# Optimization experiments

Hardware: AMD Instinct MI355X
Metric: run time of the kernel (lower is better)

The kernel has to match this reference:

```python
import jax, jax.numpy as jnp
import numpy as np

T, IN, OUT, R = 8192, 4096, 4096, 64


def setup_inputs() -> dict:
    key = jax.random.key(0)
    ks = jax.random.split(key, 7)
    # signed int4 values in [-8, 8) for activations and (unpacked) weights
    quant_x = jax.random.randint(ks[0], (T, IN), -8, 8, dtype=jnp.int32)
    weight_q = jax.random.randint(ks[1], (OUT, IN), -8, 8, dtype=jnp.int32)
    # positive per-token / per-channel symmetric-quant scales
    scale_x = jax.random.uniform(ks[2], (T,), dtype=jnp.float32) * 0.01 + 1e-4
    weight_scales = jax.random.uniform(ks[3], (OUT,), dtype=jnp.float32) * 0.01 + 1e-4
    outlier_x = jax.random.normal(ks[4], (T, R), dtype=jnp.float32)
    w_outlier = jax.random.normal(ks[5], (OUT, R), dtype=jnp.float32)
    bias = jax.random.normal(ks[6], (OUT,), dtype=jnp.float32)
    return {"quant_x": quant_x, "weight_q": weight_q, "scale_x": scale_x,
            "weight_scales": weight_scales, "outlier_x": outlier_x,
            "w_outlier": w_outlier, "bias": bias}


def reference(quant_x, weight_q, scale_x, weight_scales, outlier_x, w_outlier, bias):
    acc = jnp.matmul(quant_x, weight_q.T)
    # sym_dequant: per-row activation scale * per-column weight scale
    x_out = acc.astype(jnp.float32) * scale_x[:, None] * weight_scales[None, :]
    # outlier low-rank addmm + bias epilogue
    x_out = x_out + jnp.matmul(outlier_x, w_outlier.T) + bias
    return x_out
```

## Files before the change

### kernel.cpp

```cpp
#include <hip/hip_runtime.h>

#define T_DIM 8192
#define IN_DIM 4096
#define OUT_DIM 4096
#define R_DIM 64
#define NKT 64

typedef int i32x4 __attribute__((ext_vector_type(4)));
typedef float f32x4 __attribute__((ext_vector_type(4)));
typedef _Float16 f16x8 __attribute__((ext_vector_type(8)));

__device__ __forceinline__ int pack4(int4 v) {
  return (v.x & 255) | ((v.y & 255) << 8) | ((v.z & 255) << 16) | ((unsigned)v.w << 24);
}

__device__ __forceinline__ void gload16(const void* g, void* l) {
  __builtin_amdgcn_global_load_lds(
      (const __attribute__((address_space(1))) void*)(unsigned long long)g,
      (__attribute__((address_space(3))) void*)(unsigned)(unsigned long long)l,
      16, 0, 0);
}

__device__ __forceinline__ i32x4 unp(int x, int y) {
  i32x4 r;
  r[0] = x & 0x0F0F0F0F;
  r[1] = (x >> 4) & 0x0F0F0F0F;
  r[2] = y & 0x0F0F0F0F;
  r[3] = (y >> 4) & 0x0F0F0F0F;
  return r;
}

__device__ __forceinline__ unsigned pb(int a, int b) {
  return (unsigned)(a + 8) | ((unsigned)(b + 8) << 4);
}

__global__ __launch_bounds__(256)
void cvt_pack_kernel(const int* __restrict__ qx, const int* __restrict__ wq,
                     char* __restrict__ pk, int* __restrict__ SS) {
  const int wave = blockIdx.x * 4 + (threadIdx.x >> 6);
  const int l = threadIdx.x & 63;
  const int nw = gridDim.x * 4;
  for (int r = wave; r < T_DIM + OUT_DIM; r += nw) {
    const int* src = (r < T_DIM) ? (qx + (size_t)r * IN_DIM)
                                 : (wq + (size_t)(r - T_DIM) * IN_DIM);
    const int4* src4 = (const int4*)src;
    char* dst = pk + (size_t)r * 2048;
    const int rq = (r >> 2) & 3;
    int s = 0;
#pragma unroll
    for (int i = 0; i < 4; ++i) {
      const int idx = i * 64 + l;
      const int kt = idx >> 2, d = idx & 3;
      int4 s0 = src4[idx * 4 + 0], s1 = src4[idx * 4 + 1];
      int4 s2 = src4[idx * 4 + 2], s3 = src4[idx * 4 + 3];
      s += s0.x + s0.y + s0.z + s0.w + s1.x + s1.y + s1.z + s1.w +
           s2.x + s2.y + s2.z + s2.w + s3.x + s3.y + s3.z + s3.w;
      unsigned dw0 = pb(s0.x, s0.y) | (pb(s0.z, s0.w) << 8) |
                     (pb(s1.x, s1.y) << 16) | (pb(s1.z, s1.w) << 24);
      unsigned dw1 = pb(s2.x, s2.y) | (pb(s2.z, s2.w) << 8) |
                     (pb(s3.x, s3.y) << 16) | (pb(s3.z, s3.w) << 24);
      const int off = kt * 32 + ((d ^ rq) << 3);
      *(uint2*)(dst + off) = make_uint2(dw0, dw1);
    }
#pragma unroll
    for (int off = 1; off < 64; off <<= 1) s += __shfl_xor(s, off, 64);
    if (l == 0) SS[r] = s + 8 * IN_DIM;
  }
}

__global__ __launch_bounds__(256, 4)
void w4a4_gemm(const char* __restrict__ A8, const char* __restrict__ B8,
               const int* __restrict__ SS,
               const float* __restrict__ sx, const float* __restrict__ sw,
               const float* __restrict__ ox, const float* __restrict__ ow,
               const float* __restrict__ bias, float* __restrict__ out) {
  __shared__ __align__(16) char smem[32768];

  const int bid = blockIdx.x;
  const int xcd = bid & 7, c = bid >> 3;
  const int tn = (xcd & 3) * 8 + (c & 7);
  const int tm = (xcd >> 2) * 32 + (c >> 3);
  const int brow = tm * 128, bcol = tn * 128;

  const int t = threadIdx.x;
  const int w = t >> 6, l = t & 63;
  const int wr = w >> 1, wc = w & 1;
  const int l16 = l & 15, lk = l >> 4;
  (void)w;

  const char* gA = A8 + (size_t)(brow + (t >> 1)) * 2048 + (t & 1) * 16;
  const char* gB = B8 + (size_t)(bcol + (t >> 1)) * 2048 + (t & 1) * 16;
  char* const dA = smem + t * 16;
  char* const dB = smem + 4096 + t * 16;

  const int cho = (lk ^ ((l16 >> 2) & 3)) << 3;
  const char* aR = smem + (wr * 64 + l16) * 32 + cho;
  const char* bR = smem + 4096 + (wc * 64 + l16) * 32 + cho;

  i32x4 acc[4][4];
#pragma unroll
  for (int m = 0; m < 4; ++m)
#pragma unroll
    for (int n = 0; n < 4; ++n) acc[m][n] = (i32x4){0, 0, 0, 0};

  auto stage = [&](int kt) {
    const int off = kt << 5;
    const int buf = (kt & 3) << 13;
    gload16(gA + off, dA + buf);
    gload16(gB + off, dB + buf);
  };

  auto compute = [&](int kt) {
    const int buf = (kt & 3) << 13;
    const char* sa = aR + buf;
    const char* sb = bR + buf;
    int2 pa[4], pv[4];
#pragma unroll
    for (int m = 0; m < 4; ++m) pa[m] = *(const int2*)(sa + m * 512);
#pragma unroll
    for (int n = 0; n < 4; ++n) pv[n] = *(const int2*)(sb + n * 512);
    i32x4 bu[4];
#pragma unroll
    for (int n = 0; n < 4; ++n) bu[n] = unp(pv[n].x, pv[n].y);
    __builtin_amdgcn_s_setprio(1);
#pragma unroll
    for (int m = 0; m < 4; ++m) {
      i32x4 au = unp(pa[m].x, pa[m].y);
      acc[m][0] = __builtin_amdgcn_mfma_i32_16x16x64_i8(au, bu[0], acc[m][0], 0, 0, 0);
      acc[m][1] = __builtin_amdgcn_mfma_i32_16x16x64_i8(au, bu[1], acc[m][1], 0, 0, 0);
      acc[m][2] = __builtin_amdgcn_mfma_i32_16x16x64_i8(au, bu[2], acc[m][2], 0, 0, 0);
      acc[m][3] = __builtin_amdgcn_mfma_i32_16x16x64_i8(au, bu[3], acc[m][3], 0, 0, 0);
    }
    __builtin_amdgcn_s_setprio(0);
  };

#define VMBAR(N)                                          \
  asm volatile("s_waitcnt vmcnt(" #N ")" ::: "memory");   \
  __builtin_amdgcn_s_barrier();                           \
  __builtin_amdgcn_sched_barrier(0);

  stage(0); stage(1); stage(2);
  for (int kt = 0; kt < NKT - 3; ++kt) {
    VMBAR(4);
    stage(kt + 3);
    compute(kt);
  }
  VMBAR(4);
  compute(NKT - 3);
  VMBAR(2);
  compute(NKT - 2);
  VMBAR(0);
  compute(NKT - 1);

  const int orow0 = brow + wr * 64 + (lk << 2);
  const int ocol0 = bcol + wc * 64 + l16;
  const int* SA = SS;
  const int* SB = SS + T_DIM;
  float swv[4], bvv[4];
  int cb[4];
#pragma unroll
  for (int n = 0; n < 4; ++n) {
    swv[n] = sw[ocol0 + n * 16];
    bvv[n] = bias[ocol0 + n * 16];
    cb[n] = -8 * SB[ocol0 + n * 16];
  }

  f32x4 facc[4][4];
#pragma unroll
  for (int m = 0; m < 4; ++m) {
#pragma unroll
    for (int r = 0; r < 4; ++r) {
      const int row = orow0 + m * 16 + r;
      const float sxv = sx[row];
      const int ca = 262144 - 8 * SA[row];
#pragma unroll
      for (int n = 0; n < 4; ++n)
        facc[m][n][r] = (float)(acc[m][n][r] + ca + cb[n]) * sxv * swv[n];
    }
  }

  __syncthreads();
#pragma unroll
  for (int j = 0; j < 4; ++j) {
    int q = j * 256 + t;
    int row = q >> 3, cd = q & 7, cs = cd ^ (row & 7);
    const float* ga = ox + (size_t)(brow + row) * R_DIM + cs * 8;
    float4 f0 = *(const float4*)ga, f1 = *(const float4*)(ga + 4);
    f16x8 h;
    h[0] = (_Float16)f0.x; h[1] = (_Float16)f0.y; h[2] = (_Float16)f0.z; h[3] = (_Float16)f0.w;
    h[4] = (_Float16)f1.x; h[5] = (_Float16)f1.y; h[6] = (_Float16)f1.z; h[7] = (_Float16)f1.w;
    *(f16x8*)(smem + row * 128 + cd * 16) = h;
    const float* gb = ow + (size_t)(bcol + row) * R_DIM + cs * 8;
    f0 = *(const float4*)gb; f1 = *(const float4*)(gb + 4);
    f16x8 g;
    g[0] = (_Float16)f0.x; g[1] = (_Float16)f0.y; g[2] = (_Float16)f0.z; g[3] = (_Float16)f0.w;
    g[4] = (_Float16)f1.x; g[5] = (_Float16)f1.y; g[6] = (_Float16)f1.z; g[7] = (_Float16)f1.w;
    *(f16x8*)(smem + 16384 + row * 128 + cd * 16) = g;
  }
  __syncthreads();

  const char* qa = smem + (wr * 64 + l16) * 128;
  const char* qb = smem + 16384 + (wc * 64 + l16) * 128;
  const int x7 = l16 & 7;
#pragma unroll
  for (int s = 0; s < 2; ++s) {
    const int ca2 = ((s * 4 + lk) ^ x7) << 4;
    f16x8 hb[4];
#pragma unroll
    for (int n = 0; n < 4; ++n) hb[n] = *(const f16x8*)(qb + n * 2048 + ca2);
#pragma unroll
    for (int m = 0; m < 4; ++m) {
      f16x8 ha = *(const f16x8*)(qa + m * 2048 + ca2);
#pragma unroll
      for (int n = 0; n < 4; ++n)
        facc[m][n] = __builtin_amdgcn_mfma_f32_16x16x32_f16(ha, hb[n], facc[m][n], 0, 0, 0);
    }
  }

#pragma unroll
  for (int m = 0; m < 4; ++m)
#pragma unroll
    for (int r = 0; r < 4; ++r) {
      float* po = out + (size_t)(orow0 + m * 16 + r) * OUT_DIM + ocol0;
#pragma unroll
      for (int n = 0; n < 4; ++n) po[n * 16] = facc[m][n][r] + bvv[n];
    }
}

__global__ __launch_bounds__(256)
void w4a4_gemm_fb(const int* __restrict__ A32, const int* __restrict__ B32,
                  const float* __restrict__ sx, const float* __restrict__ sw,
                  const float* __restrict__ ox, const float* __restrict__ ow,
                  const float* __restrict__ bias, float* __restrict__ out) {
  __shared__ __align__(16) unsigned char smem[32768];
  char* sA = (char*)smem;
  char* sB = (char*)smem + 8192;

  const int bid = blockIdx.x;
  const int swzb = (bid & 7) * 256 + (bid >> 3);
  const int tm = swzb >> 5, tn = swzb & 31;
  const int brow = tm * 128, bcol = tn * 128;

  const int t = threadIdx.x;
  const int l = t & 63;
  const int wr = (t >> 6) >> 1, wc = (t >> 6) & 1;
  const int l16 = l & 15, lk = l >> 4;

  i32x4 iacc[4][4];
#pragma unroll
  for (int m = 0; m < 4; ++m)
#pragma unroll
    for (int n = 0; n < 4; ++n) iacc[m][n] = (i32x4){0, 0, 0, 0};

  const int ar = t >> 2;
  const int ac = (t & 3) << 4;
  const int* hA0 = A32 + (size_t)(brow + ar) * IN_DIM + ac;
  const int* hA1 = hA0 + (size_t)64 * IN_DIM;
  const int* hB0 = B32 + (size_t)(bcol + ar) * IN_DIM + ac;
  const int* hB1 = hB0 + (size_t)64 * IN_DIM;

  const char* fragA = sA + (size_t)(wr * 64 + l16) * 64 + lk * 16;
  const char* fragB = sB + (size_t)(wc * 64 + l16) * 64 + lk * 16;

  for (int k0 = 0; k0 < IN_DIM; k0 += 64) {
    const int4* pA0 = (const int4*)(hA0 + k0);
    int4 r0 = {pack4(pA0[0]), pack4(pA0[1]), pack4(pA0[2]), pack4(pA0[3])};
    *(int4*)(sA + t * 16) = r0;
    const int4* pA1 = (const int4*)(hA1 + k0);
    int4 r1 = {pack4(pA1[0]), pack4(pA1[1]), pack4(pA1[2]), pack4(pA1[3])};
    *(int4*)(sA + 4096 + t * 16) = r1;
    const int4* pB0 = (const int4*)(hB0 + k0);
    int4 r2 = {pack4(pB0[0]), pack4(pB0[1]), pack4(pB0[2]), pack4(pB0[3])};
    *(int4*)(sB + t * 16) = r2;
    const int4* pB1 = (const int4*)(hB1 + k0);
    int4 r3 = {pack4(pB1[0]), pack4(pB1[1]), pack4(pB1[2]), pack4(pB1[3])};
    *(int4*)(sB + 4096 + t * 16) = r3;
    __syncthreads();
    i32x4 av[4], bv[4];
#pragma unroll
    for (int m = 0; m < 4; ++m) av[m] = *(const i32x4*)(fragA + m * 1024);
#pragma unroll
    for (int n = 0; n < 4; ++n) bv[n] = *(const i32x4*)(fragB + n * 1024);
#pragma unroll
    for (int m = 0; m < 4; ++m)
#pragma unroll
      for (int n = 0; n < 4; ++n)
        iacc[m][n] = __builtin_amdgcn_mfma_i32_16x16x64_i8(av[m], bv[n], iacc[m][n], 0, 0, 0);
    __syncthreads();
  }

  const int orow = brow + wr * 64 + lk * 4;
  const int ocol = bcol + wc * 64 + l16;
  float swv[4], bvv[4];
#pragma unroll
  for (int n = 0; n < 4; ++n) { swv[n] = sw[ocol + n * 16]; bvv[n] = bias[ocol + n * 16]; }

  f32x4 facc[4][4];
#pragma unroll
  for (int m = 0; m < 4; ++m)
#pragma unroll
    for (int r = 0; r < 4; ++r) {
      float sxv = sx[orow + m * 16 + r];
#pragma unroll
      for (int n = 0; n < 4; ++n) facc[m][n][r] = (float)iacc[m][n][r] * sxv * swv[n];
    }

  _Float16* oA = (_Float16*)smem;
  _Float16* oB = (_Float16*)(smem + 16384);
#pragma unroll
  for (int j = 0; j < 4; ++j) {
    int c = j * 256 + t;
    int rr2 = c >> 3, c8 = (c & 7) << 3;
    const float* gp = ox + (size_t)(brow + rr2) * R_DIM + c8;
    float4 f0 = *(const float4*)gp;
    float4 f1 = *(const float4*)(gp + 4);
    f16x8 h;
    h[0] = (_Float16)f0.x; h[1] = (_Float16)f0.y; h[2] = (_Float16)f0.z; h[3] = (_Float16)f0.w;
    h[4] = (_Float16)f1.x; h[5] = (_Float16)f1.y; h[6] = (_Float16)f1.z; h[7] = (_Float16)f1.w;
    *(f16x8*)((char*)oA + (size_t)c * 16) = h;
    const float* gq = ow + (size_t)(bcol + rr2) * R_DIM + c8;
    f0 = *(const float4*)gq; f1 = *(const float4*)(gq + 4);
    f16x8 g;
    g[0] = (_Float16)f0.x; g[1] = (_Float16)f0.y; g[2] = (_Float16)f0.z; g[3] = (_Float16)f0.w;
    g[4] = (_Float16)f1.x; g[5] = (_Float16)f1.y; g[6] = (_Float16)f1.z; g[7] = (_Float16)f1.w;
    *(f16x8*)((char*)oB + (size_t)c * 16) = g;
  }
  __syncthreads();

  const char* qa = (const char*)oA + (size_t)(wr * 64 + l16) * 128 + lk * 16;
  const char* qb = (const char*)oB + (size_t)(wc * 64 + l16) * 128 + lk * 16;
#pragma unroll
  for (int s = 0; s < 2; ++s) {
    f16x8 ha[4], hb[4];
#pragma unroll
    for (int m = 0; m < 4; ++m) ha[m] = *(const f16x8*)(qa + m * 2048 + s * 64);
#pragma unroll
    for (int n = 0; n < 4; ++n) hb[n] = *(const f16x8*)(qb + n * 2048 + s * 64);
#pragma unroll
    for (int m = 0; m < 4; ++m)
#pragma unroll
      for (int n = 0; n < 4; ++n)
        facc[m][n] = __builtin_amdgcn_mfma_f32_16x16x32_f16(ha[m], hb[n], facc[m][n], 0, 0, 0);
  }

#pragma unroll
  for (int m = 0; m < 4; ++m)
#pragma unroll
    for (int r = 0; r < 4; ++r) {
      float* po = out + (size_t)(orow + m * 16 + r) * OUT_DIM + ocol;
#pragma unroll
      for (int n = 0; n < 4; ++n) po[n * 16] = facc[m][n][r] + bvv[n];
    }
}

extern "C" void kernel_launch(void* const* d_in, const int* in_sizes, int n_in,
                              void* d_out, int out_size, void* d_ws, size_t ws_size,
                              hipStream_t stream) {
  const int*   qx   = (const int*)d_in[0];
  const int*   wq   = (const int*)d_in[1];
  const float* sx   = (const float*)d_in[2];
  const float* sw   = (const float*)d_in[3];
  const float* ox   = (const float*)d_in[4];
  const float* ow   = (const float*)d_in[5];
  const float* bias = (const float*)d_in[6];
  float* out = (float*)d_out;

  const size_t packedA = (size_t)T_DIM * 2048;
  const size_t packedB = (size_t)OUT_DIM * 2048;
  const size_t ssBytes = (size_t)(T_DIM + OUT_DIM) * 4;
  const size_t need = packedA + packedB + ssBytes;

  if (ws_size >= need) {
    char* pk = (char*)d_ws;
    int* SS = (int*)(pk + packedA + packedB);
    cvt_pack_kernel<<<768, 256, 0, stream>>>(qx, wq, pk, SS);
    w4a4_gemm<<<2048, 256, 0, stream>>>(pk, pk + packedA, SS, sx, sw, ox, ow, bias, out);
  } else {
    w4a4_gemm_fb<<<2048, 256, 0, stream>>>(qx, wq, sx, sw, ox, ow, bias, out);
  }
}
```

Baseline: 204.2 us.

## Pre-swizzle packed operands into MFMA fragment order and load directly to registers

The pack kernel now writes the int4 operands already laid out in per-wave MFMA fragment order (64-row blocks, per k-tile), so the GEMM drops the LDS staging, barriers and async global-to-LDS pipeline. Each wave instead double-buffers global loads straight into registers. Occupancy hint drops to 2 blocks per CU. Row sums are now reduced across four blocks with atomics, which needs an extra zeroing kernel. The risk is that global-load latency and L2 traffic are no longer shared through LDS across waves, and the added launch costs time.

Measured after the change: 203.0 us. Within noise of the previous version (-0.6%).

```diff
diff --git a/kernel.cpp b/kernel.cpp
--- a/kernel.cpp
+++ b/kernel.cpp
@@ -4,7 +4,6 @@
 #define IN_DIM 4096
 #define OUT_DIM 4096
 #define R_DIM 64
-#define NKT 64
 
 typedef int i32x4 __attribute__((ext_vector_type(4)));
 typedef float f32x4 __attribute__((ext_vector_type(4)));
@@ -12,13 +11,6 @@
 
 __device__ __forceinline__ int pack4(int4 v) {
   return (v.x & 255) | ((v.y & 255) << 8) | ((v.z & 255) << 16) | ((unsigned)v.w << 24);
-}
-
-__device__ __forceinline__ void gload16(const void* g, void* l) {
-  __builtin_amdgcn_global_load_lds(
-      (const __attribute__((address_space(1))) void*)(unsigned long long)g,
-      (__attribute__((address_space(3))) void*)(unsigned)(unsigned long long)l,
-      16, 0, 0);
 }
 
 __device__ __forceinline__ i32x4 unp(int x, int y) {
@@ -34,42 +26,61 @@
   return (unsigned)(a + 8) | ((unsigned)(b + 8) << 4);
 }
 
+__global__ __launch_bounds__(1024)
+void ss_zero_kernel(int* __restrict__ SS) {
+  SS[blockIdx.x * 1024 + threadIdx.x] = 0;
+}
+
 __global__ __launch_bounds__(256)
 void cvt_pack_kernel(const int* __restrict__ qx, const int* __restrict__ wq,
                      char* __restrict__ pk, int* __restrict__ SS) {
-  const int wave = blockIdx.x * 4 + (threadIdx.x >> 6);
-  const int l = threadIdx.x & 63;
-  const int nw = gridDim.x * 4;
-  for (int r = wave; r < T_DIM + OUT_DIM; r += nw) {
-    const int* src = (r < T_DIM) ? (qx + (size_t)r * IN_DIM)
-                                 : (wq + (size_t)(r - T_DIM) * IN_DIM);
-    const int4* src4 = (const int4*)src;
-    char* dst = pk + (size_t)r * 2048;
-    const int rq = (r >> 2) & 3;
-    int s = 0;
-#pragma unroll
-    for (int i = 0; i < 4; ++i) {
-      const int idx = i * 64 + l;
-      const int kt = idx >> 2, d = idx & 3;
-      int4 s0 = src4[idx * 4 + 0], s1 = src4[idx * 4 + 1];
-      int4 s2 = src4[idx * 4 + 2], s3 = src4[idx * 4 + 3];
-      s += s0.x + s0.y + s0.z + s0.w + s1.x + s1.y + s1.z + s1.w +
-           s2.x + s2.y + s2.z + s2.w + s3.x + s3.y + s3.z + s3.w;
-      unsigned dw0 = pb(s0.x, s0.y) | (pb(s0.z, s0.w) << 8) |
-                     (pb(s1.x, s1.y) << 16) | (pb(s1.z, s1.w) << 24);
-      unsigned dw1 = pb(s2.x, s2.y) | (pb(s2.z, s2.w) << 8) |
-                     (pb(s3.x, s3.y) << 16) | (pb(s3.z, s3.w) << 24);
-      const int off = kt * 32 + ((d ^ rq) << 3);
-      *(uint2*)(dst + off) = make_uint2(dw0, dw1);
-    }
-#pragma unroll
-    for (int off = 1; off < 64; off <<= 1) s += __shfl_xor(s, off, 64);
-    if (l == 0) SS[r] = s + 8 * IN_DIM;
-  }
-}
-
-__global__ __launch_bounds__(256, 4)
-void w4a4_gemm(const char* __restrict__ A8, const char* __restrict__ B8,
+  const int rb = blockIdx.x >> 2;
+  const int q = blockIdx.x & 3;
+  const int w = threadIdx.x >> 6, l = threadIdx.x & 63;
+  const int l16 = l & 15, lk = l >> 4;
+
+  const int* src = (rb < 128) ? (qx + (size_t)rb * 64 * IN_DIM)
+                              : (wq + (size_t)(rb - 128) * 64 * IN_DIM);
+  char* dst = pk + (size_t)rb * 131072;
+
+  int s[4] = {0, 0, 0, 0};
+#pragma unroll
+  for (int j = 0; j < 4; ++j) {
+    const int kt = q * 16 + w * 4 + j;
+#pragma unroll
+    for (int m = 0; m < 4; ++m) {
+      const int row = m * 16 + l16;
+      const int4* ip = (const int4*)((const char*)src + (size_t)row * 16384 + kt * 256 + lk * 64);
+      int4 v0 = ip[0], v1 = ip[1], v2 = ip[2], v3 = ip[3];
+      s[m] += v0.x + v0.y + v0.z + v0.w + v1.x + v1.y + v1.z + v1.w +
+              v2.x + v2.y + v2.z + v2.w + v3.x + v3.y + v3.z + v3.w;
+      unsigned dw0 = pb(v0.x, v0.y) | (pb(v0.z, v0.w) << 8) |
+                     (pb(v1.x, v1.y) << 16) | (pb(v1.z, v1.w) << 24);
+      unsigned dw1 = pb(v2.x, v2.y) | (pb(v2.z, v2.w) << 8) |
+                     (pb(v3.x, v3.y) << 16) | (pb(v3.z, v3.w) << 24);
+      *(uint2*)(dst + kt * 2048 + m * 512 + l * 8) = make_uint2(dw0, dw1);
+    }
+  }
+
+  __shared__ int sPart[256];
+#pragma unroll
+  for (int m = 0; m < 4; ++m) {
+    int v = s[m];
+    v += __shfl_xor(v, 16, 64);
+    v += __shfl_xor(v, 32, 64);
+    if (l < 16) sPart[w * 64 + m * 16 + l] = v;
+  }
+  __syncthreads();
+  const int t = threadIdx.x;
+  if (t < 64) {
+    int tot = sPart[t] + sPart[64 + t] + sPart[128 + t] + sPart[192 + t];
+    if (q == 0) tot += 8 * IN_DIM;
+    atomicAdd(&SS[rb * 64 + t], tot);
+  }
+}
+
+__global__ __launch_bounds__(256, 2)
+void w4a4_gemm(const char* __restrict__ A2, const char* __restrict__ B2,
                const int* __restrict__ SS,
                const float* __restrict__ sx, const float* __restrict__ sw,
                const float* __restrict__ ox, const float* __restrict__ ow,
@@ -86,16 +97,9 @@
   const int w = t >> 6, l = t & 63;
   const int wr = w >> 1, wc = w & 1;
   const int l16 = l & 15, lk = l >> 4;
-  (void)w;
-
-  const char* gA = A8 + (size_t)(brow + (t >> 1)) * 2048 + (t & 1) * 16;
-  const char* gB = B8 + (size_t)(bcol + (t >> 1)) * 2048 + (t & 1) * 16;
-  char* const dA = smem + t * 16;
-  char* const dB = smem + 4096 + t * 16;
-
-  const int cho = (lk ^ ((l16 >> 2) & 3)) << 3;
-  const char* aR = smem + (wr * 64 + l16) * 32 + cho;
-  const char* bR = smem + 4096 + (wc * 64 + l16) * 32 + cho;
+
+  const char* aP = A2 + (size_t)(tm * 2 + wr) * 131072 + l * 8;
+  const char* bP = B2 + (size_t)(tn * 2 + wc) * 131072 + l * 8;
 
   i32x4 acc[4][4];
 #pragma unroll
@@ -103,54 +107,50 @@
 #pragma unroll
     for (int n = 0; n < 4; ++n) acc[m][n] = (i32x4){0, 0, 0, 0};
 
-  auto stage = [&](int kt) {
-    const int off = kt << 5;
-    const int buf = (kt & 3) << 13;
-    gload16(gA + off, dA + buf);
-    gload16(gB + off, dB + buf);
-  };
-
-  auto compute = [&](int kt) {
-    const int buf = (kt & 3) << 13;
-    const char* sa = aR + buf;
-    const char* sb = bR + buf;
-    int2 pa[4], pv[4];
-#pragma unroll
-    for (int m = 0; m < 4; ++m) pa[m] = *(const int2*)(sa + m * 512);
-#pragma unroll
-    for (int n = 0; n < 4; ++n) pv[n] = *(const int2*)(sb + n * 512);
-    i32x4 bu[4];
-#pragma unroll
-    for (int n = 0; n < 4; ++n) bu[n] = unp(pv[n].x, pv[n].y);
-    __builtin_amdgcn_s_setprio(1);
-#pragma unroll
-    for (int m = 0; m < 4; ++m) {
-      i32x4 au = unp(pa[m].x, pa[m].y);
-      acc[m][0] = __builtin_amdgcn_mfma_i32_16x16x64_i8(au, bu[0], acc[m][0], 0, 0, 0);
-      acc[m][1] = __builtin_amdgcn_mfma_i32_16x16x64_i8(au, bu[1], acc[m][1], 0, 0, 0);
-      acc[m][2] = __builtin_amdgcn_mfma_i32_16x16x64_i8(au, bu[2], acc[m][2], 0, 0, 0);
-      acc[m][3] = __builtin_amdgcn_mfma_i32_16x16x64_i8(au, bu[3], acc[m][3], 0, 0, 0);
-    }
-    __builtin_amdgcn_s_setprio(0);
-  };
-
-#define VMBAR(N)                                          \
-  asm volatile("s_waitcnt vmcnt(" #N ")" ::: "memory");   \
-  __builtin_amdgcn_s_barrier();                           \
-  __builtin_amdgcn_sched_barrier(0);
-
-  stage(0); stage(1); stage(2);
-  for (int kt = 0; kt < NKT - 3; ++kt) {
-    VMBAR(4);
-    stage(kt + 3);
-    compute(kt);
-  }
-  VMBAR(4);
-  compute(NKT - 3);
-  VMBAR(2);
-  compute(NKT - 2);
-  VMBAR(0);
-  compute(NKT - 1);
+#define LDA(D, KT)                                                     \
+  {                                                                    \
+    const char* p_ = aP + (size_t)(KT) * 2048;                         \
+    D[0] = *(const uint2*)(p_);                                        \
+    D[1] = *(const uint2*)(p_ + 512);                                  \
+    D[2] = *(const uint2*)(p_ + 1024);                                 \
+    D[3] = *(const uint2*)(p_ + 1536);                                 \
+  }
+#define LDB(D, KT)                                                     \
+  {                                                                    \
+    const char* p_ = bP + (size_t)(KT) * 2048;                         \
+    D[0] = *(const uint2*)(p_);                                        \
+    D[1] = *(const uint2*)(p_ + 512);                                  \
+    D[2] = *(const uint2*)(p_ + 1024);                                 \
+    D[3] = *(const uint2*)(p_ + 1536);                                 \
+  }
+#define COMPUTE(AS, BS)                                                \
+  {                                                                    \
+    i32x4 bv0 = unp(BS[0].x, BS[0].y);                                 \
+    i32x4 bv1 = unp(BS[1].x, BS[1].y);                                 \
+    i32x4 bv2 = unp(BS[2].x, BS[2].y);                                 \
+    i32x4 bv3 = unp(BS[3].x, BS[3].y);                                 \
+    __builtin_amdgcn_s_setprio(1);                                     \
+    _Pragma("unroll")                                                  \
+    for (int m_ = 0; m_ < 4; ++m_) {                                   \
+      i32x4 av = unp(AS[m_].x, AS[m_].y);                              \
+      acc[m_][0] = __builtin_amdgcn_mfma_i32_16x16x64_i8(av, bv0, acc[m_][0], 0, 0, 0); \
+      acc[m_][1] = __builtin_amdgcn_mfma_i32_16x16x64_i8(av, bv1, acc[m_][1], 0, 0, 0); \
+      acc[m_][2] = __builtin_amdgcn_mfma_i32_16x16x64_i8(av, bv2, acc[m_][2], 0, 0, 0); \
+      acc[m_][3] = __builtin_amdgcn_mfma_i32_16x16x64_i8(av, bv3, acc[m_][3], 0, 0, 0); \
+    }                                                                  \
+    __builtin_amdgcn_s_setprio(0);                                     \
+  }
+
+  uint2 a0[4], b0[4], a1[4], b1[4];
+  LDA(a0, 0) LDB(b0, 0)
+  LDA(a1, 1) LDB(b1, 1)
+
+  for (int kt = 0; kt < 64; kt += 2) {
+    COMPUTE(a0, b0);
+    if (kt + 2 < 64) { LDA(a0, kt + 2) LDB(b0, kt + 2) }
+    COMPUTE(a1, b1);
+    if (kt + 3 < 64) { LDA(a1, kt + 3) LDB(b1, kt + 3) }
+  }
 
   const int orow0 = brow + wr * 64 + (lk << 2);
   const int ocol0 = bcol + wc * 64 + l16;
@@ -373,6 +373,7 @@
   if (ws_size >= need) {
     char* pk = (char*)d_ws;
     int* SS = (int*)(pk + packedA + packedB);
+    ss_zero_kernel<<<12, 1024, 0, stream>>>(SS);
     cvt_pack_kernel<<<768, 256, 0, stream>>>(qx, wq, pk, SS);
     w4a4_gemm<<<2048, 256, 0, stream>>>(pk, pk + packedA, SS, sx, sw, ox, ow, bias, out);
   } else {
```
